# Optimization experiments

Measured on AMD Instinct MI355X. Metric: run time of the kernel, lower is better.

The kernel has to match this reference:

```python
import jax, jax.numpy as jnp
import numpy as np
import math

N_WIRES = 8
DIM = 2 ** N_WIRES  # 256

# Pauli-Z sign table: wire 0 is the most-significant axis of the statevector.
_idx = np.arange(DIM)
_SIGNS = np.stack([1.0 - 2.0 * ((_idx >> (N_WIRES - 1 - w)) & 1) for w in range(N_WIRES)], axis=1).astype(np.float32)  # [256, 8]


def _cnot(state, c, t):
    # state: [N, 2, 2, ..., 2]; flip target axis where control bit == 1
    s0, s1 = jnp.split(state, 2, axis=1 + c)
    s1 = jnp.flip(s1, axis=1 + t)
    return jnp.concatenate([s0, s1], axis=1 + c)


def _quantum_heads(x, theta):
    """Simulate the QLayer circuit. x: [N, 8] -> PauliZ expectations [N, 8].

    Circuit: RX(x_i) then RX(theta_i) on wire i (commute -> RX(x_i+theta_i)),
    CNOT chain (0,1)...(6,7),(7,0), MeasureAll(PauliZ).
    """
    phi = 0.5 * (x + theta)  # RX half-angle
    c = jnp.cos(phi)
    s = jnp.sin(phi)
    # RX(a)|0> = cos(a/2)|0> - i sin(a/2)|1>
    amps = jax.lax.complex(jnp.stack([c, jnp.zeros_like(c)], axis=-1),
                           jnp.stack([jnp.zeros_like(s), -s], axis=-1))  # [N, 8, 2] complex64
    # Product state as rank-8 tensor [N, 2, ..., 2]
    state = amps[:, 0]
    for w in range(1, N_WIRES):
        state = state[..., None] * amps[:, w].reshape((-1,) + (1,) * w + (2,))
    # Entangling CNOT ring
    for w in range(N_WIRES - 1):
        state = _cnot(state, w, w + 1)
    state = _cnot(state, N_WIRES - 1, 0)
    probs = jnp.abs(state.reshape(-1, DIM)) ** 2  # [N, 256]
    return probs @ jnp.asarray(_SIGNS)  # [N, 8]


def setup_inputs() -> dict:
    key = jax.random.key(0)
    k1, k2, k3, k4 = jax.random.split(key, 4)
    B, S, E = 32, 512, 64
    return {
        "x": jax.random.normal(k1, (B, S, E), dtype=jnp.float32),
        "theta": jax.random.normal(k2, (N_WIRES,), dtype=jnp.float32),
        "W": jax.random.normal(k3, (E, E), dtype=jnp.float32) * 0.05,
        "b": jax.random.normal(k4, (E,), dtype=jnp.float32) * 0.05,
    }


def reference(x, theta, W, b):
    B, S, E = x.shape
    H = E // N_WIRES  # num_heads
    # q = k = v: same deterministic quantum projection applied to the same x.
    z = _quantum_heads(x.reshape(B * S * H, N_WIRES), theta).reshape(B, S, H, N_WIRES)
    scale = 1.0 / math.sqrt(E // H)
    # NOTE: matmul over last dims -> attention across heads within each token.
    scores = jnp.einsum('bshd,bstd->bsht', z, z) * scale  # [B, S, H, H]
    attn = jax.nn.softmax(scores, axis=-1)
    out = jnp.einsum('bsht,bstd->bshd', attn, z).reshape(B, S, E)
    return out @ W.T + b
```

## Files before the change

### kernel.cpp

```cpp
#include <hip/hip_runtime.h>


#define TOK_PER_BLK 32

typedef __attribute__((ext_vector_type(8))) short short8;
typedef __attribute__((ext_vector_type(4))) float f32x4;

__device__ inline unsigned short f2bf(float f) {
    unsigned u = __float_as_uint(f);
    u += 0x7FFF + ((u >> 16) & 1);
    return (unsigned short)(u >> 16);
}

__global__ __launch_bounds__(256, 2)
void mhaq_fused3(const float* __restrict__ x,
                 const float* __restrict__ theta,
                 const float* __restrict__ W,
                 const float* __restrict__ bias,
                 float* __restrict__ out,
                 int n_tokens)
{
    __shared__ __align__(16) unsigned short Ws[64 * 72];
    __shared__ __align__(16) float          zs[TOK_PER_BLK * 68];
    __shared__ __align__(16) unsigned short os[TOK_PER_BLK * 72];
    __shared__ float bs[64];

    const int tid = threadIdx.x;
    const int tl  = tid >> 3;
    const int g   = tid & 7;
    const int token = blockIdx.x * TOK_PER_BLK + tl;
    const bool valid = token < n_tokens;

    {
        const float4* __restrict__ Wv = reinterpret_cast<const float4*>(W);
        #pragma unroll
        for (int i = 0; i < 4; ++i) {
            int idx = i * 256 + tid;
            int j   = idx >> 4;
            int c4  = idx & 15;
            float4 w = Wv[idx];
            *reinterpret_cast<ushort4*>(&Ws[j * 72 + c4 * 4]) =
                make_ushort4(f2bf(w.x), f2bf(w.y), f2bf(w.z), f2bf(w.w));
        }
        if (tid < 16)
            reinterpret_cast<float4*>(bs)[tid] =
                reinterpret_cast<const float4*>(bias)[tid];
    }

    float zh[8];
    {
        float4 a  = make_float4(0.f, 0.f, 0.f, 0.f);
        float4 b4 = make_float4(0.f, 0.f, 0.f, 0.f);
        if (valid) {
            const float4* __restrict__ xp =
                reinterpret_cast<const float4*>(x) + (size_t)token * 16 + g * 2;
            a = xp[0]; b4 = xp[1];
        }
        float c0 = __cosf(a.x  + theta[0]);
        float c1 = __cosf(a.y  + theta[1]);
        float c2 = __cosf(a.z  + theta[2]);
        float c3 = __cosf(a.w  + theta[3]);
        float c4 = __cosf(b4.x + theta[4]);
        float c5 = __cosf(b4.y + theta[5]);
        float c6 = __cosf(b4.z + theta[6]);
        float c7 = __cosf(b4.w + theta[7]);
        float p1 = c0 * c1;
        float p2 = p1 * c2;
        float p3 = p2 * c3;
        float p4 = p3 * c4;
        float p5 = p4 * c5;
        float p6 = p5 * c6;
        float p7 = p6 * c7;
        float s6 = c6 * c7;
        float s5 = c5 * s6;
        float s4 = c4 * s5;
        float s3 = c3 * s4;
        float s2 = c2 * s3;
        float s1 = c1 * s2;
        zh[0] = s1; zh[1] = p1; zh[2] = p2; zh[3] = p3;
        zh[4] = p4; zh[5] = p5; zh[6] = p6; zh[7] = p7;

        float4* z4 = reinterpret_cast<float4*>(zs + tl * 68 + g * 8);
        z4[0] = make_float4(zh[0], zh[1], zh[2], zh[3]);
        z4[1] = make_float4(zh[4], zh[5], zh[6], zh[7]);
    }
    __syncthreads();

    {
        __align__(16) float zf[64];
        const float* zrow = zs + tl * 68;
        #pragma unroll
        for (int k4 = 0; k4 < 16; ++k4)
            *reinterpret_cast<float4*>(&zf[4 * k4]) =
                *reinterpret_cast<const float4*>(&zrow[4 * k4]);

        const float scale = 0.35355339059327373f;
        float sc[8];
        float m = -4.0f;
        #pragma unroll
        for (int t = 0; t < 8; ++t) {
            float s = 0.f;
            #pragma unroll
            for (int d = 0; d < 8; ++d)
                s = fmaf(zh[d], zf[t * 8 + d], s);
            s *= scale;
            sc[t] = s;
            m = fmaxf(m, s);
        }
        float sum = 0.f;
        #pragma unroll
        for (int t = 0; t < 8; ++t) {
            sc[t] = __expf(sc[t] - m);
            sum += sc[t];
        }
        float inv = 1.0f / sum;

        unsigned short oh[8];
        #pragma unroll
        for (int d = 0; d < 8; ++d) {
            float acc = 0.f;
            #pragma unroll
            for (int t = 0; t < 8; ++t)
                acc = fmaf(sc[t], zf[t * 8 + d], acc);
            oh[d] = f2bf(acc * inv);
        }
        ushort4* o4 = reinterpret_cast<ushort4*>(&os[tl * 72 + g * 8]);
        o4[0] = make_ushort4(oh[0], oh[1], oh[2], oh[3]);
        o4[1] = make_ushort4(oh[4], oh[5], oh[6], oh[7]);
    }
    __syncthreads();

    {
        const int lane = tid & 63;
        const int wave = tid >> 6;
        const int mt   = wave & 1;
        const int np   = wave >> 1;
        const int lr   = lane & 15;
        const int lg   = lane >> 4;

        short8 bfrag[2][2];
        #pragma unroll
        for (int nt = 0; nt < 2; ++nt) {
            int j = np * 32 + nt * 16 + lr;
            #pragma unroll
            for (int kt = 0; kt < 2; ++kt)
                bfrag[nt][kt] = *reinterpret_cast<const short8*>(
                    &Ws[j * 72 + kt * 32 + lg * 8]);
        }
        short8 afrag[2];
        #pragma unroll
        for (int kt = 0; kt < 2; ++kt)
            afrag[kt] = *reinterpret_cast<const short8*>(
                &os[(mt * 16 + lr) * 72 + kt * 32 + lg * 8]);

        #pragma unroll
        for (int nt = 0; nt < 2; ++nt) {
            int j = np * 32 + nt * 16 + lr;
            float bj = bs[j];
            f32x4 acc = {bj, bj, bj, bj};
            #pragma unroll
            for (int kt = 0; kt < 2; ++kt)
                acc = __builtin_amdgcn_mfma_f32_16x16x32_bf16(
                    afrag[kt], bfrag[nt][kt], acc, 0, 0, 0);
            #pragma unroll
            for (int r = 0; r < 4; ++r) {
                int trow = blockIdx.x * TOK_PER_BLK + mt * 16 + lg * 4 + r;
                if (trow < n_tokens)
                    out[(size_t)trow * 64 + j] = acc[r];
            }
        }
    }
}

extern "C" void kernel_launch(void* const* d_in, const int* in_sizes, int n_in,
                              void* d_out, int out_size, void* d_ws, size_t ws_size,
                              hipStream_t stream)
{
    const float* x     = (const float*)d_in[0];
    const float* theta = (const float*)d_in[1];
    const float* W     = (const float*)d_in[2];
    const float* b     = (const float*)d_in[3];
    float* out         = (float*)d_out;

    const int n_tokens = in_sizes[0] / 64;
    const int blocks   = (n_tokens + TOK_PER_BLK - 1) / TOK_PER_BLK;
    mhaq_fused3<<<blocks, 256, 0, stream>>>(x, theta, W, b, out, n_tokens);
}
```

Before: 9.805 us.

## Load W fragments straight to registers and shrink blocks to 16 tokens

Removes the shared-memory staging of W and bias: each wave loads its MFMA B-fragments of W directly from global memory into registers and converts them to bf16 right before the MFMA. Blocks shrink to 16 tokens and 128 threads, so there are twice as many blocks, each with less shared memory. The softmax max-subtraction is dropped because the scores are bounded. Each block now reads its W slice from global/L2 with no sharing across waves, so total W traffic rises.

Measured after the change: 9.858 us. About the same (+0.5%).

```diff
diff --git a/kernel.cpp b/kernel.cpp
--- a/kernel.cpp
+++ b/kernel.cpp
@@ -1,7 +1,7 @@
 #include <hip/hip_runtime.h>
 
 
-#define TOK_PER_BLK 32
+#define TOK_PER_BLK 16
 
 typedef __attribute__((ext_vector_type(8))) short short8;
 typedef __attribute__((ext_vector_type(4))) float f32x4;
@@ -12,41 +12,54 @@
     return (unsigned short)(u >> 16);
 }
 
-__global__ __launch_bounds__(256, 2)
-void mhaq_fused3(const float* __restrict__ x,
+__device__ inline short8 pack_bf16x8(float4 a, float4 b) {
+    short8 r;
+    r[0] = (short)f2bf(a.x); r[1] = (short)f2bf(a.y);
+    r[2] = (short)f2bf(a.z); r[3] = (short)f2bf(a.w);
+    r[4] = (short)f2bf(b.x); r[5] = (short)f2bf(b.y);
+    r[6] = (short)f2bf(b.z); r[7] = (short)f2bf(b.w);
+    return r;
+}
+
+__global__ __launch_bounds__(128, 2)
+void mhaq_fused4(const float* __restrict__ x,
                  const float* __restrict__ theta,
                  const float* __restrict__ W,
                  const float* __restrict__ bias,
                  float* __restrict__ out,
                  int n_tokens)
 {
-    __shared__ __align__(16) unsigned short Ws[64 * 72];
     __shared__ __align__(16) float          zs[TOK_PER_BLK * 68];
     __shared__ __align__(16) unsigned short os[TOK_PER_BLK * 72];
-    __shared__ float bs[64];
 
-    const int tid = threadIdx.x;
-    const int tl  = tid >> 3;
-    const int g   = tid & 7;
-    const int token = blockIdx.x * TOK_PER_BLK + tl;
-    const bool valid = token < n_tokens;
+    const int tid  = threadIdx.x;
+    const int lane = tid & 63;
+    const int wave = tid >> 6;
+    const int lr   = lane & 15;
+    const int lg   = lane >> 4;
+    const int blockbase = blockIdx.x * TOK_PER_BLK;
 
+    float4 wf[2][2][2];
+    float  bj[2];
     {
         const float4* __restrict__ Wv = reinterpret_cast<const float4*>(W);
         #pragma unroll
-        for (int i = 0; i < 4; ++i) {
-            int idx = i * 256 + tid;
-            int j   = idx >> 4;
-            int c4  = idx & 15;
-            float4 w = Wv[idx];
-            *reinterpret_cast<ushort4*>(&Ws[j * 72 + c4 * 4]) =
-                make_ushort4(f2bf(w.x), f2bf(w.y), f2bf(w.z), f2bf(w.w));
+        for (int nt = 0; nt < 2; ++nt) {
+            int j = wave * 32 + nt * 16 + lr;
+            bj[nt] = bias[j];
+            #pragma unroll
+            for (int kt = 0; kt < 2; ++kt) {
+                int fidx = (j * 64 + kt * 32 + lg * 8) >> 2;
+                wf[nt][kt][0] = Wv[fidx];
+                wf[nt][kt][1] = Wv[fidx + 1];
+            }
         }
-        if (tid < 16)
-            reinterpret_cast<float4*>(bs)[tid] =
-                reinterpret_cast<const float4*>(bias)[tid];
     }
 
+    const int tl = tid >> 3;
+    const int g  = tid & 7;
+    const int token = blockbase + tl;
+    const bool valid = token < n_tokens;
     float zh[8];
     {
         float4 a  = make_float4(0.f, 0.f, 0.f, 0.f);
@@ -96,23 +109,16 @@
 
         const float scale = 0.35355339059327373f;
         float sc[8];
-        float m = -4.0f;
         #pragma unroll
         for (int t = 0; t < 8; ++t) {
             float s = 0.f;
             #pragma unroll
             for (int d = 0; d < 8; ++d)
                 s = fmaf(zh[d], zf[t * 8 + d], s);
-            s *= scale;
-            sc[t] = s;
-            m = fmaxf(m, s);
+            sc[t] = __expf(s * scale);
         }
-        float sum = 0.f;
-        #pragma unroll
-        for (int t = 0; t < 8; ++t) {
-            sc[t] = __expf(sc[t] - m);
-            sum += sc[t];
-        }
+        float sum = sc[0] + sc[1] + sc[2] + sc[3]
+                  + sc[4] + sc[5] + sc[6] + sc[7];
         float inv = 1.0f / sum;
 
         unsigned short oh[8];
@@ -131,40 +137,25 @@
     __syncthreads();
 
     {
-        const int lane = tid & 63;
-        const int wave = tid >> 6;
-        const int mt   = wave & 1;
-        const int np   = wave >> 1;
-        const int lr   = lane & 15;
-        const int lg   = lane >> 4;
-
-        short8 bfrag[2][2];
-        #pragma unroll
-        for (int nt = 0; nt < 2; ++nt) {
-            int j = np * 32 + nt * 16 + lr;
-            #pragma unroll
-            for (int kt = 0; kt < 2; ++kt)
-                bfrag[nt][kt] = *reinterpret_cast<const short8*>(
-                    &Ws[j * 72 + kt * 32 + lg * 8]);
-        }
         short8 afrag[2];
         #pragma unroll
         for (int kt = 0; kt < 2; ++kt)
             afrag[kt] = *reinterpret_cast<const short8*>(
-                &os[(mt * 16 + lr) * 72 + kt * 32 + lg * 8]);
+                &os[lr * 72 + kt * 32 + lg * 8]);
 
         #pragma unroll
         for (int nt = 0; nt < 2; ++nt) {
-            int j = np * 32 + nt * 16 + lr;
-            float bj = bs[j];
-            f32x4 acc = {bj, bj, bj, bj};
+            int j = wave * 32 + nt * 16 + lr;
+            f32x4 acc = {bj[nt], bj[nt], bj[nt], bj[nt]};
             #pragma unroll
-            for (int kt = 0; kt < 2; ++kt)
+            for (int kt = 0; kt < 2; ++kt) {
+                short8 bfrag = pack_bf16x8(wf[nt][kt][0], wf[nt][kt][1]);
                 acc = __builtin_amdgcn_mfma_f32_16x16x32_bf16(
-                    afrag[kt], bfrag[nt][kt], acc, 0, 0, 0);
+                    afrag[kt], bfrag, acc, 0, 0, 0);
+            }
             #pragma unroll
             for (int r = 0; r < 4; ++r) {
-                int trow = blockIdx.x * TOK_PER_BLK + mt * 16 + lg * 4 + r;
+                int trow = blockbase + lg * 4 + r;
                 if (trow < n_tokens)
                     out[(size_t)trow * 64 + j] = acc[r];
             }
@@ -184,5 +175,5 @@
 
     const int n_tokens = in_sizes[0] / 64;
     const int blocks   = (n_tokens + TOK_PER_BLK - 1) / TOK_PER_BLK;
-    mhaq_fused3<<<blocks, 256, 0, stream>>>(x, theta, W, b, out, n_tokens);
+    mhaq_fused4<<<blocks, 128, 0, stream>>>(x, theta, W, b, out, n_tokens);
 }
```
